# Optimization experiments

Measured on AMD Instinct MI355X. Metric: run time of the kernel, lower is better.

The kernel has to match this reference:

```python
import jax, jax.numpy as jnp
import numpy as np

C_IN, H, W, B = 8, 40, 40, 4

def _build_static():
    # mirrors FlexChannelPConv2D.__init__ precomputation (all static / non-trainable)
    inp_rot = np.zeros(C_IN, dtype=np.int64)
    out_rot = np.repeat(np.arange(3), 12)                      # [36]
    rings    = np.array([0.0, 1.0, 2.0])                       # kernel_size=5 -> radii 0..2
    ring_sig = np.array([0.6, 0.6, 0.4])
    out_ext = np.concatenate([out_rot, -out_rot])              # complex_mode=False appends -out_rot
    freqs_all = np.unique(out_ext[:, None] - inp_rot[None, :]) # [-2..2]
    basis = [(r, s, f) for r, s in zip(rings, ring_sig)
             for f in freqs_all if (abs(f) <= r or f == 0)]    # bandlimit filter
    b_rad = np.array([b[0] for b in basis], np.float32)
    b_sig = np.array([b[1] for b in basis], np.float32)
    b_frq = np.array([b[2] for b in basis], np.float32)
    F = len(basis)
    pre_inp = np.repeat(inp_rot, F).astype(np.float64)         # meshgrid(inp_rot, freq) flattened, c-major
    pre_flt = np.tile(b_frq.astype(np.float64), C_IN)
    pre_out = pre_inp + pre_flt
    pre_mul = np.stack([np.ones_like(pre_out), np.sign(pre_out + 0.5)], -1)
    m0 = pre_inp == 0
    pre_mul[m0] *= 0.5 * (np.sign(pre_out[m0])[:, None] + 1)
    pre_mul[pre_out == 0] *= 2
    pre_out = np.abs(pre_out)
    conn = pre_out[:, None] == out_rot[None, :]                # [C*F, C_out]
    pre_cut = (pre_mul != 0).any(1) & conn.any(1)
    pre_mul = pre_mul[pre_cut]
    conn = conn[pre_cut]
    rows, cols = np.nonzero(conn)                              # row-major, matches torch bool-mask assign
    return dict(b_rad=b_rad, b_sig=b_sig, b_frq=b_frq,
                pre_cut_idx=np.nonzero(pre_cut)[0].astype(np.int32),
                pre_mul=pre_mul.astype(np.float32),
                conn_rows=rows.astype(np.int32), conn_cols=cols.astype(np.int32),
                out_rot=out_rot.astype(np.int32))

def setup_inputs() -> dict:
    key = jax.random.key(0)
    st = _build_static()
    k1, k2 = jax.random.split(key)
    data = jax.random.normal(k1, (B, H * W, C_IN), jnp.float32)
    gy, gx = jnp.meshgrid(jnp.arange(H, dtype=jnp.float32) - (H - 1) / 2.0,
                          jnp.arange(W, dtype=jnp.float32) - (W - 1) / 2.0,
                          indexing='ij')
    inp_grid = jnp.stack([gy, gx], 0)                          # [2,H,W]
    nnz = st['conn_rows'].shape[0]
    weights = jax.random.normal(k2, (nnz, 2), jnp.float32) * (2.0 / nnz) ** 0.5
    return dict(data=data, inp_grid=inp_grid, weights=weights,
                basis_radius=jnp.asarray(st['b_rad']),
                basis_sigma=jnp.asarray(st['b_sig']),
                basis_frequency=jnp.asarray(st['b_frq']),
                pre_mul=jnp.asarray(st['pre_mul']),
                pre_cut_idx=jnp.asarray(st['pre_cut_idx']),
                conn_rows=jnp.asarray(st['conn_rows']),
                conn_cols=jnp.asarray(st['conn_cols']),
                out_rot=jnp.asarray(st['out_rot']))

def reference(data, inp_grid, weights, basis_radius, basis_sigma, basis_frequency,
              pre_mul, pre_cut_idx, conn_rows, conn_cols, out_rot):
    g = inp_grid.reshape(2, -1)                                # [2,P]  (unpad=0 -> out_grid == inp_grid)
    coords = g[:, :, None] - g[:, None, :]                     # [2,P,Q]
    radius = jnp.sqrt(coords[0] ** 2 + coords[1] ** 2)[..., None]   # [P,Q,1]
    angles = jnp.arctan2(coords[0], coords[1])[..., None]           # [P,Q,1]
    re = -((radius - basis_radius) / (2.0 ** 0.5 * basis_sigma)) ** 2
    im = angles * basis_frequency
    mask = (radius != 0) | (basis_frequency == 0)
    pre_filter = jnp.exp(jax.lax.complex(re, im)) * mask       # [P,Q,F] complex64
    datac = data.astype(jnp.complex64)
    pp = jnp.einsum('bpc,pqf->bqcf', datac, pre_filter)        # [B,Q,C,F]
    Bn, Q = pp.shape[0], pp.shape[1]
    pp = pp.reshape(Bn, Q, -1)[..., pre_cut_idx]               # [B,Q,Fsel]
    pp = jax.lax.complex(pp.real * pre_mul[:, 0], pp.imag * pre_mul[:, 1])
    Fsel = pre_cut_idx.shape[0]
    Cout = out_rot.shape[0]
    wfull = jnp.zeros((Fsel, Cout), jnp.complex64).at[conn_rows, conn_cols].set(
        jax.lax.complex(weights[:, 0], weights[:, 1]))
    out = jnp.einsum('bqf,fc->bqc', pp, wfull)                 # [B,Q,Cout] complex
    keep_imag = (out_rot != 0).astype(out.real.dtype)
    out = jax.lax.complex(out.real, out.imag * keep_imag)      # zero imag on freq-0 outputs
    return jnp.stack([out.real, out.imag], -1)                 # real view [B,Q,Cout,2]
```

## Files before the change

kernel.cpp:

```cpp
#include <hip/hip_runtime.h>


#define HGRID 40
#define WGRID 40
#define NP    1600
#define NB    4
#define NC    8
#define COUT  36
#define NNZ   576
#define FSEL  48
#define WIN   4
#define WTAB  9
#define MAXROW 24

__global__ __launch_bounds__(512)
void flexpconv_kernel(const float* __restrict__ data,
                      const float* __restrict__ weights,
                      const float* __restrict__ brad,
                      const float* __restrict__ bsig,
                      const float* __restrict__ premul,
                      const int*   __restrict__ conn_rows,
                      const int*   __restrict__ conn_cols,
                      const int*   __restrict__ out_rot,
                      float*       __restrict__ out)
{
    __shared__ float tab[WTAB * WTAB][8];
    __shared__ float ppbuf[8][FSEL][2];
    __shared__ int   colRow[MAXROW][COUT];
    __shared__ float colWre[MAXROW][COUT];
    __shared__ float colWim[MAXROW][COUT];
    __shared__ int   colCnt[COUT];

    const int tid = threadIdx.x;

    if (tid < COUT) colCnt[tid] = 0;
    if (tid < WTAB * WTAB) {
        const int dy = tid / WTAB - WIN;
        const int dx = tid % WTAB - WIN;
        const float fy = (float)dy, fx = (float)dx;
        const float r2 = fy * fy + fx * fx;
        const float r  = sqrtf(r2);
        const float inv_s2 = 0.70710678118654752f;
        const float R0 = brad[0], S0 = bsig[0];
        const float R1 = brad[1], S1 = bsig[1];
        const float R2 = brad[4], S2 = bsig[4];
        float t0 = (r - R0) * inv_s2 / S0;
        float t1 = (r - R1) * inv_s2 / S1;
        float t2 = (r - R2) * inv_s2 / S2;
        float e0 = expf(-t0 * t0);
        float e1 = expf(-t1 * t1);
        float e2 = expf(-t2 * t2);
        float c1 = 0.f, s1 = 0.f, c2v = 0.f, s2v = 0.f;
        if (r2 > 0.f) {
            const float ir = 1.f / r;
            c1 = fx * ir;
            s1 = fy * ir;
            c2v = c1 * c1 - s1 * s1;
            s2v = 2.f * c1 * s1;
        }
        tab[tid][0] = e0; tab[tid][1] = e1; tab[tid][2] = e2; tab[tid][3] = c1;
        tab[tid][4] = s1; tab[tid][5] = c2v; tab[tid][6] = s2v; tab[tid][7] = 0.f;
    }
    __syncthreads();

    for (int n = tid; n < NNZ; n += 512) {
        const int col  = conn_cols[n];
        const int slot = atomicAdd(&colCnt[col], 1);
        colRow[slot][col] = conn_rows[n];
        colWre[slot][col] = weights[2 * n];
        colWim[slot][col] = weights[2 * n + 1];
    }

    const int c    = tid & 7;
    const int b    = (tid >> 3) & 3;
    const int half = (tid >> 5) & 1;
    const int ql   = tid >> 6;
    const int q    = blockIdx.x * 8 + ql;
    const int qy   = q / WGRID;
    const int qx   = q - qy * WGRID;

    float p0 = 0.f, p1 = 0.f, p3 = 0.f;
    float p2r = 0.f, p2i = 0.f;
    float p4r = 0.f, p4i = 0.f;
    float p5r = 0.f, p5i = 0.f;

    const int dy_lo = half ? 1 : -WIN;
    const int dy_hi = half ? WIN : 0;
    for (int dy = dy_lo; dy <= dy_hi; ++dy) {
        const int py = qy + dy;
        if (py < 0 || py >= HGRID) continue;
        const int rowbase = (b * NP + py * WGRID) * NC + c;
        const int obase   = (dy + WIN) * WTAB;
        #pragma unroll
        for (int dx = -WIN; dx <= WIN; ++dx) {
            const int px = qx + dx;
            if (px < 0 || px >= WGRID) continue;
            const float4 tA = *(const float4*)&tab[obase + dx + WIN][0];
            const float4 tB = *(const float4*)&tab[obase + dx + WIN][4];
            const float d = data[rowbase + px * NC];
            p0 += d * tA.x;
            p1 += d * tA.y;
            p3 += d * tA.z;
            const float dc1 = d * tA.w, ds1 = d * tB.x;
            const float dc2 = d * tB.y, ds2 = d * tB.z;
            p2r += dc1 * tA.y; p2i += ds1 * tA.y;
            p4r += dc1 * tA.z; p4i += ds1 * tA.z;
            p5r += dc2 * tA.z; p5i += ds2 * tA.z;
        }
    }

    p0  += __shfl_xor(p0, 32);  p1  += __shfl_xor(p1, 32);
    p3  += __shfl_xor(p3, 32);
    p2r += __shfl_xor(p2r, 32); p2i += __shfl_xor(p2i, 32);
    p4r += __shfl_xor(p4r, 32); p4i += __shfl_xor(p4i, 32);
    p5r += __shfl_xor(p5r, 32); p5i += __shfl_xor(p5i, 32);

    if (half == 0) {
        const int kb = c * 6;
        float* dst = &ppbuf[ql][0][0];
        (void)dst;
    }
    __shared__ float ppb[8][NB][FSEL][2];
    if (half == 0) {
        const int kb = c * 6;
        ppb[ql][b][kb + 0][0] = p0  * premul[(kb + 0) * 2];
        ppb[ql][b][kb + 0][1] = 0.f;
        ppb[ql][b][kb + 1][0] = p1  * premul[(kb + 1) * 2];
        ppb[ql][b][kb + 1][1] = 0.f;
        ppb[ql][b][kb + 2][0] = p2r * premul[(kb + 2) * 2];
        ppb[ql][b][kb + 2][1] = p2i * premul[(kb + 2) * 2 + 1];
        ppb[ql][b][kb + 3][0] = p3  * premul[(kb + 3) * 2];
        ppb[ql][b][kb + 3][1] = 0.f;
        ppb[ql][b][kb + 4][0] = p4r * premul[(kb + 4) * 2];
        ppb[ql][b][kb + 4][1] = p4i * premul[(kb + 4) * 2 + 1];
        ppb[ql][b][kb + 5][0] = p5r * premul[(kb + 5) * 2];
        ppb[ql][b][kb + 5][1] = p5i * premul[(kb + 5) * 2 + 1];
    }
    __syncthreads();

    const int r_  = tid & 63;
    const int eb  = r_ >> 4;
    const int l16 = r_ & 15;
    #pragma unroll
    for (int cc = 0; cc < 3; ++cc) {
        const int co = cc * 16 + l16;
        if (co >= COUT) continue;
        const int cnt = colCnt[co];
        float are = 0.f, aim = 0.f;
        for (int i = 0; i < cnt; ++i) {
            const int k  = colRow[i][co];
            const float wr = colWre[i][co];
            const float wi = colWim[i][co];
            const float pr = ppb[ql][eb][k][0];
            const float pi = ppb[ql][eb][k][1];
            are += pr * wr - pi * wi;
            aim += pr * wi + pi * wr;
        }
        if (out_rot[co] == 0) aim = 0.f;
        const int oidx = ((eb * NP + q) * COUT + co) * 2;
        out[oidx]     = are;
        out[oidx + 1] = aim;
    }
}

extern "C" void kernel_launch(void* const* d_in, const int* in_sizes, int n_in,
                              void* d_out, int out_size, void* d_ws, size_t ws_size,
                              hipStream_t stream) {
    const float* data      = (const float*)d_in[0];
    const float* weights   = (const float*)d_in[2];
    const float* brad      = (const float*)d_in[3];
    const float* bsig      = (const float*)d_in[4];
    const float* premul    = (const float*)d_in[6];
    const int*   conn_rows = (const int*)d_in[8];
    const int*   conn_cols = (const int*)d_in[9];
    const int*   out_rot   = (const int*)d_in[10];
    float* out = (float*)d_out;

    flexpconv_kernel<<<NP / 8, 512, 0, stream>>>(
        data, weights, brad, bsig, premul, conn_rows, conn_cols, out_rot, out);
}
```

Baseline: 85.47 us.

## Split weight-table build into a prologue kernel and use one block per output point

Moves the per-block CSC weight gather into a separate single-block init kernel that writes padded column tables to workspace. The main kernel now runs 1600 blocks of 256 threads, one query point per block. Within a block, all 81 taps are spread across 8 lane groups and reduced with xor shuffles, and the contraction loop runs a fixed 24 rows per column read from global memory. This removes the redundant atomic table build in every block and raises the number of blocks. In exchange it adds a second launch, repeats the table setup in 1600 blocks, and spends extra work on zero-padded rows.

```diff
diff --git a/kernel.cpp b/kernel.cpp
--- a/kernel.cpp
+++ b/kernel.cpp
@@ -3,7 +3,7 @@
 
 #define HGRID 40
 #define WGRID 40
-#define NP    1600
+#define NQ    1600
 #define NB    4
 #define NC    8
 #define COUT  36
@@ -11,30 +11,50 @@
 #define FSEL  48
 #define WIN   4
 #define WTAB  9
+#define NTAP  81
 #define MAXROW 24
 
-__global__ __launch_bounds__(512)
-void flexpconv_kernel(const float* __restrict__ data,
-                      const float* __restrict__ weights,
-                      const float* __restrict__ brad,
-                      const float* __restrict__ bsig,
-                      const float* __restrict__ premul,
-                      const int*   __restrict__ conn_rows,
-                      const int*   __restrict__ conn_cols,
-                      const int*   __restrict__ out_rot,
-                      float*       __restrict__ out)
+__global__ __launch_bounds__(576)
+void flex_init_wtab(const float* __restrict__ weights,
+                    const int*   __restrict__ conn_rows,
+                    const int*   __restrict__ conn_cols,
+                    int*   __restrict__ wrow,
+                    float* __restrict__ wre,
+                    float* __restrict__ wim)
 {
-    __shared__ float tab[WTAB * WTAB][8];
-    __shared__ float ppbuf[8][FSEL][2];
-    __shared__ int   colRow[MAXROW][COUT];
-    __shared__ float colWre[MAXROW][COUT];
-    __shared__ float colWim[MAXROW][COUT];
-    __shared__ int   colCnt[COUT];
+    __shared__ int cnt[COUT];
+    const int tid = threadIdx.x;
+    if (tid < COUT) cnt[tid] = 0;
+    for (int i = tid; i < MAXROW * COUT; i += 576) {
+        wrow[i] = 0; wre[i] = 0.f; wim[i] = 0.f;
+    }
+    __syncthreads();
+    if (tid < NNZ) {
+        const int col  = conn_cols[tid];
+        const int slot = atomicAdd(&cnt[col], 1);
+        wrow[slot * COUT + col] = conn_rows[tid];
+        wre [slot * COUT + col] = weights[2 * tid];
+        wim [slot * COUT + col] = weights[2 * tid + 1];
+    }
+}
+
+__global__ __launch_bounds__(256)
+void flex_main(const float* __restrict__ data,
+               const float* __restrict__ brad,
+               const float* __restrict__ bsig,
+               const float* __restrict__ premul,
+               const int*   __restrict__ out_rot,
+               const int*   __restrict__ wrow,
+               const float* __restrict__ wre,
+               const float* __restrict__ wim,
+               float*       __restrict__ out)
+{
+    __shared__ float tab[NTAP][8];
+    __shared__ float ppb[NB][FSEL][2];
 
     const int tid = threadIdx.x;
 
-    if (tid < COUT) colCnt[tid] = 0;
-    if (tid < WTAB * WTAB) {
+    if (tid < NTAP) {
         const int dy = tid / WTAB - WIN;
         const int dx = tid % WTAB - WIN;
         const float fy = (float)dy, fx = (float)dx;
@@ -44,60 +64,52 @@
         const float R0 = brad[0], S0 = bsig[0];
         const float R1 = brad[1], S1 = bsig[1];
         const float R2 = brad[4], S2 = bsig[4];
-        float t0 = (r - R0) * inv_s2 / S0;
-        float t1 = (r - R1) * inv_s2 / S1;
-        float t2 = (r - R2) * inv_s2 / S2;
-        float e0 = expf(-t0 * t0);
-        float e1 = expf(-t1 * t1);
-        float e2 = expf(-t2 * t2);
+        const float t0 = (r - R0) * inv_s2 / S0;
+        const float t1 = (r - R1) * inv_s2 / S1;
+        const float t2 = (r - R2) * inv_s2 / S2;
+        const float e0 = expf(-t0 * t0);
+        const float e1 = expf(-t1 * t1);
+        const float e2 = expf(-t2 * t2);
         float c1 = 0.f, s1 = 0.f, c2v = 0.f, s2v = 0.f;
         if (r2 > 0.f) {
             const float ir = 1.f / r;
-            c1 = fx * ir;
-            s1 = fy * ir;
+            c1 = fx * ir; s1 = fy * ir;
             c2v = c1 * c1 - s1 * s1;
             s2v = 2.f * c1 * s1;
         }
-        tab[tid][0] = e0; tab[tid][1] = e1; tab[tid][2] = e2; tab[tid][3] = c1;
-        tab[tid][4] = s1; tab[tid][5] = c2v; tab[tid][6] = s2v; tab[tid][7] = 0.f;
+        tab[tid][0] = e0;  tab[tid][1] = e1;  tab[tid][2] = e2;  tab[tid][3] = c1;
+        tab[tid][4] = s1;  tab[tid][5] = c2v; tab[tid][6] = s2v; tab[tid][7] = 0.f;
     }
     __syncthreads();
 
-    for (int n = tid; n < NNZ; n += 512) {
-        const int col  = conn_cols[n];
-        const int slot = atomicAdd(&colCnt[col], 1);
-        colRow[slot][col] = conn_rows[n];
-        colWre[slot][col] = weights[2 * n];
-        colWim[slot][col] = weights[2 * n + 1];
-    }
+    const int q  = blockIdx.x;
+    const int qy = q / WGRID;
+    const int qx = q - qy * WGRID;
 
-    const int c    = tid & 7;
-    const int b    = (tid >> 3) & 3;
-    const int half = (tid >> 5) & 1;
-    const int ql   = tid >> 6;
-    const int q    = blockIdx.x * 8 + ql;
-    const int qy   = q / WGRID;
-    const int qx   = q - qy * WGRID;
+    const int b    = tid >> 6;
+    const int lane = tid & 63;
+    const int c    = lane & 7;
+    const int tg   = lane >> 3;
 
     float p0 = 0.f, p1 = 0.f, p3 = 0.f;
     float p2r = 0.f, p2i = 0.f;
     float p4r = 0.f, p4i = 0.f;
     float p5r = 0.f, p5i = 0.f;
 
-    const int dy_lo = half ? 1 : -WIN;
-    const int dy_hi = half ? WIN : 0;
-    for (int dy = dy_lo; dy <= dy_hi; ++dy) {
-        const int py = qy + dy;
-        if (py < 0 || py >= HGRID) continue;
-        const int rowbase = (b * NP + py * WGRID) * NC + c;
-        const int obase   = (dy + WIN) * WTAB;
-        #pragma unroll
-        for (int dx = -WIN; dx <= WIN; ++dx) {
+    const int base_bc = b * NQ * NC + c;
+    #pragma unroll
+    for (int round = 0; round < 11; ++round) {
+        const int t = tg + round * 8;
+        if (t < NTAP) {
+            const int dy = t / WTAB - WIN;
+            const int dx = t - (dy + WIN) * WTAB - WIN;
+            const int py = qy + dy;
             const int px = qx + dx;
-            if (px < 0 || px >= WGRID) continue;
-            const float4 tA = *(const float4*)&tab[obase + dx + WIN][0];
-            const float4 tB = *(const float4*)&tab[obase + dx + WIN][4];
-            const float d = data[rowbase + px * NC];
+            const bool ok = (py >= 0) & (py < HGRID) & (px >= 0) & (px < WGRID);
+            float d = 0.f;
+            if (ok) d = data[base_bc + (py * WGRID + px) * NC];
+            const float4 tA = *(const float4*)&tab[t][0];
+            const float4 tB = *(const float4*)&tab[t][4];
             p0 += d * tA.x;
             p1 += d * tA.y;
             p3 += d * tA.z;
@@ -109,57 +121,45 @@
         }
     }
 
-    p0  += __shfl_xor(p0, 32);  p1  += __shfl_xor(p1, 32);
-    p3  += __shfl_xor(p3, 32);
-    p2r += __shfl_xor(p2r, 32); p2i += __shfl_xor(p2i, 32);
-    p4r += __shfl_xor(p4r, 32); p4i += __shfl_xor(p4i, 32);
-    p5r += __shfl_xor(p5r, 32); p5i += __shfl_xor(p5i, 32);
+    #pragma unroll
+    for (int m = 8; m <= 32; m <<= 1) {
+        p0  += __shfl_xor(p0, m);  p1  += __shfl_xor(p1, m);
+        p3  += __shfl_xor(p3, m);
+        p2r += __shfl_xor(p2r, m); p2i += __shfl_xor(p2i, m);
+        p4r += __shfl_xor(p4r, m); p4i += __shfl_xor(p4i, m);
+        p5r += __shfl_xor(p5r, m); p5i += __shfl_xor(p5i, m);
+    }
 
-    if (half == 0) {
+    if (tg == 0) {
         const int kb = c * 6;
-        float* dst = &ppbuf[ql][0][0];
-        (void)dst;
-    }
-    __shared__ float ppb[8][NB][FSEL][2];
-    if (half == 0) {
-        const int kb = c * 6;
-        ppb[ql][b][kb + 0][0] = p0  * premul[(kb + 0) * 2];
-        ppb[ql][b][kb + 0][1] = 0.f;
-        ppb[ql][b][kb + 1][0] = p1  * premul[(kb + 1) * 2];
-        ppb[ql][b][kb + 1][1] = 0.f;
-        ppb[ql][b][kb + 2][0] = p2r * premul[(kb + 2) * 2];
-        ppb[ql][b][kb + 2][1] = p2i * premul[(kb + 2) * 2 + 1];
-        ppb[ql][b][kb + 3][0] = p3  * premul[(kb + 3) * 2];
-        ppb[ql][b][kb + 3][1] = 0.f;
-        ppb[ql][b][kb + 4][0] = p4r * premul[(kb + 4) * 2];
-        ppb[ql][b][kb + 4][1] = p4i * premul[(kb + 4) * 2 + 1];
-        ppb[ql][b][kb + 5][0] = p5r * premul[(kb + 5) * 2];
-        ppb[ql][b][kb + 5][1] = p5i * premul[(kb + 5) * 2 + 1];
+        ppb[b][kb + 0][0] = p0  * premul[(kb + 0) * 2];  ppb[b][kb + 0][1] = 0.f;
+        ppb[b][kb + 1][0] = p1  * premul[(kb + 1) * 2];  ppb[b][kb + 1][1] = 0.f;
+        ppb[b][kb + 2][0] = p2r * premul[(kb + 2) * 2];
+        ppb[b][kb + 2][1] = p2i * premul[(kb + 2) * 2 + 1];
+        ppb[b][kb + 3][0] = p3  * premul[(kb + 3) * 2];  ppb[b][kb + 3][1] = 0.f;
+        ppb[b][kb + 4][0] = p4r * premul[(kb + 4) * 2];
+        ppb[b][kb + 4][1] = p4i * premul[(kb + 4) * 2 + 1];
+        ppb[b][kb + 5][0] = p5r * premul[(kb + 5) * 2];
+        ppb[b][kb + 5][1] = p5i * premul[(kb + 5) * 2 + 1];
     }
     __syncthreads();
 
-    const int r_  = tid & 63;
-    const int eb  = r_ >> 4;
-    const int l16 = r_ & 15;
-    #pragma unroll
-    for (int cc = 0; cc < 3; ++cc) {
-        const int co = cc * 16 + l16;
-        if (co >= COUT) continue;
-        const int cnt = colCnt[co];
+    const int co = lane;
+    if (co < COUT) {
         float are = 0.f, aim = 0.f;
-        for (int i = 0; i < cnt; ++i) {
-            const int k  = colRow[i][co];
-            const float wr = colWre[i][co];
-            const float wi = colWim[i][co];
-            const float pr = ppb[ql][eb][k][0];
-            const float pi = ppb[ql][eb][k][1];
+        #pragma unroll 4
+        for (int i = 0; i < MAXROW; ++i) {
+            const int   k  = wrow[i * COUT + co];
+            const float wr = wre [i * COUT + co];
+            const float wi = wim [i * COUT + co];
+            const float pr = ppb[b][k][0];
+            const float pi = ppb[b][k][1];
             are += pr * wr - pi * wi;
             aim += pr * wi + pi * wr;
         }
         if (out_rot[co] == 0) aim = 0.f;
-        const int oidx = ((eb * NP + q) * COUT + co) * 2;
-        out[oidx]     = are;
-        out[oidx + 1] = aim;
+        float2* o2 = (float2*)out;
+        o2[(b * NQ + q) * COUT + co] = make_float2(are, aim);
     }
 }
 
@@ -176,6 +176,12 @@
     const int*   out_rot   = (const int*)d_in[10];
     float* out = (float*)d_out;
 
-    flexpconv_kernel<<<NP / 8, 512, 0, stream>>>(
-        data, weights, brad, bsig, premul, conn_rows, conn_cols, out_rot, out);
+    int*   wrow = (int*)d_ws;
+    float* wre  = (float*)((char*)d_ws + MAXROW * COUT * sizeof(int));
+    float* wim  = (float*)((char*)d_ws + 2 * MAXROW * COUT * sizeof(int));
+
+    flex_init_wtab<<<1, 576, 0, stream>>>(weights, conn_rows, conn_cols,
+                                          wrow, wre, wim);
+    flex_main<<<NQ, 256, 0, stream>>>(data, brad, bsig, premul, out_rot,
+                                      wrow, wre, wim, out);
 }
```

Result: no change. 86.00 us (+0.6%).
